# Kernel tuning notes

Measured on AMD Instinct MI355X. Metric: run time of the kernel, lower is better.

The kernel has to match this reference:

```python
import jax, jax.numpy as jnp
import numpy as np

N = 262144  # number of candidate occluded-object feature rows

def _w(k, shape, fan_in):
    return jax.random.normal(k, shape, jnp.float32) * (1.0 / np.sqrt(fan_in))

def setup_inputs() -> dict:
    key = jax.random.key(0)
    ks = jax.random.split(key, 5)
    return {
        "select_feature": jax.random.normal(ks[0], (N, 512), jnp.float32),
        # Conv2d(512,256,1x1) == Linear(512->256); Conv2d(256,128,1x1) == Linear(256->128)
        "W1": _w(ks[1], (256, 512), 512), "b1": jnp.zeros((256,), jnp.float32),
        "W2": _w(ks[2], (128, 256), 256), "b2": jnp.zeros((128,), jnp.float32),
        "Wf1": _w(ks[3], (64, 128), 128), "bf1": jnp.zeros((64,), jnp.float32),
        "Wf2": _w(ks[4], (2, 64), 64),   "bf2": jnp.zeros((2,), jnp.float32),
    }

def reference(select_feature, W1, b1, W2, b2, Wf1, bf1, Wf2, bf2):
    # masker_train: unsqueeze->1x1 convs->squeeze is exactly a per-row MLP.
    h = jax.nn.relu(select_feature @ W1.T + b1)   # [N,256]
    h = jax.nn.relu(h @ W2.T + b2)                # [N,128]
    h = jax.nn.relu(h @ Wf1.T + bf1)              # [N,64]
    logits = h @ Wf2.T + bf2                      # [N,2]
    return jax.nn.softmax(logits, axis=-1)
```

## Files before the change

kernel.cpp:

```cpp
#include <hip/hip_runtime.h>
#include <hip/hip_bf16.h>

typedef __bf16 bf16x8 __attribute__((ext_vector_type(8)));
typedef float  f32x4  __attribute__((ext_vector_type(4)));

#define MFMA16(a, b, c) __builtin_amdgcn_mfma_f32_16x16x32_bf16((a), (b), (c), 0, 0, 0)

__global__ void prep_weights(const float* __restrict__ W1, const float* __restrict__ W2,
                             const float* __restrict__ Wf1, const float* __restrict__ Wf2,
                             __bf16* __restrict__ w1p, __bf16* __restrict__ w2p,
                             __bf16* __restrict__ wf1p, __bf16* __restrict__ wf2b) {
    int t = blockIdx.x * 256 + threadIdx.x;
    int lane = t & 63, m16 = lane & 15, q = (lane >> 4) & 3;
    if (t < 16384) {
        int ct = (t >> 6) & 15, ks = t >> 10;
        const float* s = W1 + (size_t)(ct * 16 + m16) * 512 + ks * 32 + q * 8;
        __bf16* d = w1p + (size_t)t * 8;
        for (int j = 0; j < 8; ++j) d[j] = (__bf16)s[j];
    }
    if (t < 4096) {
        int ct = (t >> 6) & 7, ks = t >> 9;
        const float* s = W2 + (size_t)(ct * 16 + m16) * 256 + ks * 32 + q * 8;
        __bf16* d = w2p + (size_t)t * 8;
        for (int j = 0; j < 8; ++j) d[j] = (__bf16)s[j];
    }
    if (t < 1024) {
        int ct = (t >> 6) & 3, ks = t >> 8;
        const float* s = Wf1 + (size_t)(ct * 16 + m16) * 128 + ks * 32 + q * 8;
        __bf16* d = wf1p + (size_t)t * 8;
        for (int j = 0; j < 8; ++j) d[j] = (__bf16)s[j];
    }
    if (t < 128) wf2b[t] = (__bf16)Wf2[t];
}

__global__ __launch_bounds__(128, 2)
void mlp_kernel(const float* __restrict__ X,
                const __bf16* __restrict__ w1p,  const float* __restrict__ b1,
                const __bf16* __restrict__ w2p,  const float* __restrict__ b2,
                const __bf16* __restrict__ wf1p, const float* __restrict__ bf1,
                const __bf16* __restrict__ wf2b, const float* __restrict__ bf2,
                float* __restrict__ out) {
    __shared__ __align__(16) __bf16 hbuf[2][32][264];

    const int lane = threadIdx.x & 63;
    const int wave = threadIdx.x >> 6;
    const int m16  = lane & 15;
    const int q    = lane >> 4;
    const int row0 = blockIdx.x * 64 + wave * 32;
    __bf16(*hw)[264] = hbuf[wave];

    f32x4 C1[2][16];
#pragma unroll
    for (int rt = 0; rt < 2; ++rt)
#pragma unroll
        for (int ct = 0; ct < 16; ++ct) C1[rt][ct] = (f32x4){0.f, 0.f, 0.f, 0.f};

    const float* xr0 = X + (size_t)(row0 + m16) * 512 + q * 8;
    const float* xr1 = xr0 + (size_t)16 * 512;
    float4 x00 = *(const float4*)(xr0);
    float4 x01 = *(const float4*)(xr0 + 4);
    float4 x10 = *(const float4*)(xr1);
    float4 x11 = *(const float4*)(xr1 + 4);

#pragma unroll
    for (int ks = 0; ks < 16; ++ks) {
        const __bf16* wp = w1p + (size_t)ks * 8192 + lane * 8;
        bf16x8 b0[8], b1v[8];
#pragma unroll
        for (int ct = 0; ct < 8; ++ct)
            b0[ct] = *(const bf16x8*)(wp + ct * 512);

        bf16x8 a0, a1;
        a0[0] = (__bf16)x00.x; a0[1] = (__bf16)x00.y; a0[2] = (__bf16)x00.z; a0[3] = (__bf16)x00.w;
        a0[4] = (__bf16)x01.x; a0[5] = (__bf16)x01.y; a0[6] = (__bf16)x01.z; a0[7] = (__bf16)x01.w;
        a1[0] = (__bf16)x10.x; a1[1] = (__bf16)x10.y; a1[2] = (__bf16)x10.z; a1[3] = (__bf16)x10.w;
        a1[4] = (__bf16)x11.x; a1[5] = (__bf16)x11.y; a1[6] = (__bf16)x11.z; a1[7] = (__bf16)x11.w;

        if (ks < 15) {
            x00 = *(const float4*)(xr0 + (ks + 1) * 32);
            x01 = *(const float4*)(xr0 + (ks + 1) * 32 + 4);
            x10 = *(const float4*)(xr1 + (ks + 1) * 32);
            x11 = *(const float4*)(xr1 + (ks + 1) * 32 + 4);
        }
#pragma unroll
        for (int ct = 0; ct < 8; ++ct)
            b1v[ct] = *(const bf16x8*)(wp + (8 + ct) * 512);

#pragma unroll
        for (int ct = 0; ct < 8; ++ct) {
            C1[0][ct] = MFMA16(a0, b0[ct], C1[0][ct]);
            C1[1][ct] = MFMA16(a1, b0[ct], C1[1][ct]);
        }
#pragma unroll
        for (int ct = 0; ct < 8; ++ct) {
            C1[0][8 + ct] = MFMA16(a0, b1v[ct], C1[0][8 + ct]);
            C1[1][8 + ct] = MFMA16(a1, b1v[ct], C1[1][8 + ct]);
        }
    }
#pragma unroll
    for (int ct = 0; ct < 16; ++ct) {
        float bias = b1[ct * 16 + m16];
#pragma unroll
        for (int rt = 0; rt < 2; ++rt)
#pragma unroll
            for (int r = 0; r < 4; ++r) {
                float v = C1[rt][ct][r] + bias;
                v = v > 0.f ? v : 0.f;
                hw[rt * 16 + q * 4 + r][ct * 16 + m16] = (__bf16)v;
            }
    }

    f32x4 C2[2][8];
#pragma unroll
    for (int rt = 0; rt < 2; ++rt)
#pragma unroll
        for (int ct = 0; ct < 8; ++ct) C2[rt][ct] = (f32x4){0.f, 0.f, 0.f, 0.f};

#pragma unroll
    for (int ks = 0; ks < 8; ++ks) {
        const __bf16* wp = w2p + (size_t)ks * 4096 + lane * 8;
        bf16x8 b[8];
#pragma unroll
        for (int ct = 0; ct < 8; ++ct) b[ct] = *(const bf16x8*)(wp + ct * 512);
        bf16x8 a0 = *(const bf16x8*)&hw[m16][ks * 32 + q * 8];
        bf16x8 a1 = *(const bf16x8*)&hw[16 + m16][ks * 32 + q * 8];
#pragma unroll
        for (int ct = 0; ct < 8; ++ct) {
            C2[0][ct] = MFMA16(a0, b[ct], C2[0][ct]);
            C2[1][ct] = MFMA16(a1, b[ct], C2[1][ct]);
        }
    }
#pragma unroll
    for (int ct = 0; ct < 8; ++ct) {
        float bias = b2[ct * 16 + m16];
#pragma unroll
        for (int rt = 0; rt < 2; ++rt)
#pragma unroll
            for (int r = 0; r < 4; ++r) {
                float v = C2[rt][ct][r] + bias;
                v = v > 0.f ? v : 0.f;
                hw[rt * 16 + q * 4 + r][ct * 16 + m16] = (__bf16)v;
            }
    }

    f32x4 C3[2][4];
#pragma unroll
    for (int rt = 0; rt < 2; ++rt)
#pragma unroll
        for (int ct = 0; ct < 4; ++ct) C3[rt][ct] = (f32x4){0.f, 0.f, 0.f, 0.f};

#pragma unroll
    for (int ks = 0; ks < 4; ++ks) {
        const __bf16* wp = wf1p + (size_t)ks * 2048 + lane * 8;
        bf16x8 b[4];
#pragma unroll
        for (int ct = 0; ct < 4; ++ct) b[ct] = *(const bf16x8*)(wp + ct * 512);
        bf16x8 a0 = *(const bf16x8*)&hw[m16][ks * 32 + q * 8];
        bf16x8 a1 = *(const bf16x8*)&hw[16 + m16][ks * 32 + q * 8];
#pragma unroll
        for (int ct = 0; ct < 4; ++ct) {
            C3[0][ct] = MFMA16(a0, b[ct], C3[0][ct]);
            C3[1][ct] = MFMA16(a1, b[ct], C3[1][ct]);
        }
    }
#pragma unroll
    for (int ct = 0; ct < 4; ++ct) {
        float bias = bf1[ct * 16 + m16];
#pragma unroll
        for (int rt = 0; rt < 2; ++rt)
#pragma unroll
            for (int r = 0; r < 4; ++r) {
                float v = C3[rt][ct][r] + bias;
                v = v > 0.f ? v : 0.f;
                hw[rt * 16 + q * 4 + r][ct * 16 + m16] = (__bf16)v;
            }
    }

    {
        const int r = lane >> 1;
        const int c = lane & 1;
        float dot = 0.f;
#pragma unroll
        for (int j8 = 0; j8 < 8; ++j8) {
            bf16x8 hv = *(const bf16x8*)&hw[r][j8 * 8];
            bf16x8 wv = *(const bf16x8*)(wf2b + c * 64 + j8 * 8);
#pragma unroll
            for (int j = 0; j < 8; ++j) dot += (float)hv[j] * (float)wv[j];
        }
        float logit = dot + bf2[c];
        float other = __shfl_xor(logit, 1, 64);
        float mx = fmaxf(logit, other);
        float e0 = expf(logit - mx);
        float e1 = expf(other - mx);
        out[(size_t)(row0 + r) * 2 + c] = e0 / (e0 + e1);
    }
}

extern "C" void kernel_launch(void* const* d_in, const int* in_sizes, int n_in,
                              void* d_out, int out_size, void* d_ws, size_t ws_size,
                              hipStream_t stream) {
    const float* X   = (const float*)d_in[0];
    const float* W1  = (const float*)d_in[1];
    const float* b1  = (const float*)d_in[2];
    const float* W2  = (const float*)d_in[3];
    const float* b2  = (const float*)d_in[4];
    const float* Wf1 = (const float*)d_in[5];
    const float* bf1 = (const float*)d_in[6];
    const float* Wf2 = (const float*)d_in[7];
    const float* bf2 = (const float*)d_in[8];
    float* out = (float*)d_out;

    const int N = in_sizes[0] / 512;

    __bf16* w1p  = (__bf16*)d_ws;
    __bf16* w2p  = w1p  + 131072;
    __bf16* wf1p = w2p  + 32768;
    __bf16* wf2b = wf1p + 8192;

    prep_weights<<<64, 256, 0, stream>>>(W1, W2, Wf1, Wf2, w1p, w2p, wf1p, wf2b);
    mlp_kernel<<<N / 64, 128, 0, stream>>>(X, w1p, b1, w2p, b2, wf1p, bf1,
                                           wf2b, bf2, out);
}
```

Baseline: 797.9 us.

## Use 4-wave blocks with per-k-step barriers and nontemporal X loads and stores

The block grows from 2 to 4 waves (128 rows), with matching shared memory. An s_barrier is added at every k-step of all three MFMA loops, so the waves stay in lockstep and share the weight fetches in L1/L2. The streaming input loads and the output stores become nontemporal so X does not pollute the cache. The barriers add synchronisation stalls, and launch_bounds(256,2) may tighten the register budget for the large accumulator arrays.

```diff
diff --git a/kernel.cpp b/kernel.cpp
--- a/kernel.cpp
+++ b/kernel.cpp
@@ -5,6 +5,10 @@
 typedef float  f32x4  __attribute__((ext_vector_type(4)));
 
 #define MFMA16(a, b, c) __builtin_amdgcn_mfma_f32_16x16x32_bf16((a), (b), (c), 0, 0, 0)
+
+__device__ __forceinline__ f32x4 nt_load4(const float* p) {
+    return __builtin_nontemporal_load((const f32x4*)p);
+}
 
 __global__ void prep_weights(const float* __restrict__ W1, const float* __restrict__ W2,
                              const float* __restrict__ Wf1, const float* __restrict__ Wf2,
@@ -33,20 +37,20 @@
     if (t < 128) wf2b[t] = (__bf16)Wf2[t];
 }
 
-__global__ __launch_bounds__(128, 2)
+__global__ __launch_bounds__(256, 2)
 void mlp_kernel(const float* __restrict__ X,
                 const __bf16* __restrict__ w1p,  const float* __restrict__ b1,
                 const __bf16* __restrict__ w2p,  const float* __restrict__ b2,
                 const __bf16* __restrict__ wf1p, const float* __restrict__ bf1,
                 const __bf16* __restrict__ wf2b, const float* __restrict__ bf2,
                 float* __restrict__ out) {
-    __shared__ __align__(16) __bf16 hbuf[2][32][264];
+    __shared__ __align__(16) __bf16 hbuf[4][32][264];
 
     const int lane = threadIdx.x & 63;
     const int wave = threadIdx.x >> 6;
     const int m16  = lane & 15;
     const int q    = lane >> 4;
-    const int row0 = blockIdx.x * 64 + wave * 32;
+    const int row0 = blockIdx.x * 128 + wave * 32;
     __bf16(*hw)[264] = hbuf[wave];
 
     f32x4 C1[2][16];
@@ -57,13 +61,14 @@
 
     const float* xr0 = X + (size_t)(row0 + m16) * 512 + q * 8;
     const float* xr1 = xr0 + (size_t)16 * 512;
-    float4 x00 = *(const float4*)(xr0);
-    float4 x01 = *(const float4*)(xr0 + 4);
-    float4 x10 = *(const float4*)(xr1);
-    float4 x11 = *(const float4*)(xr1 + 4);
+    f32x4 x00 = nt_load4(xr0);
+    f32x4 x01 = nt_load4(xr0 + 4);
+    f32x4 x10 = nt_load4(xr1);
+    f32x4 x11 = nt_load4(xr1 + 4);
 
 #pragma unroll
     for (int ks = 0; ks < 16; ++ks) {
+        __builtin_amdgcn_s_barrier();
         const __bf16* wp = w1p + (size_t)ks * 8192 + lane * 8;
         bf16x8 b0[8], b1v[8];
 #pragma unroll
@@ -71,16 +76,16 @@
             b0[ct] = *(const bf16x8*)(wp + ct * 512);
 
         bf16x8 a0, a1;
-        a0[0] = (__bf16)x00.x; a0[1] = (__bf16)x00.y; a0[2] = (__bf16)x00.z; a0[3] = (__bf16)x00.w;
-        a0[4] = (__bf16)x01.x; a0[5] = (__bf16)x01.y; a0[6] = (__bf16)x01.z; a0[7] = (__bf16)x01.w;
-        a1[0] = (__bf16)x10.x; a1[1] = (__bf16)x10.y; a1[2] = (__bf16)x10.z; a1[3] = (__bf16)x10.w;
-        a1[4] = (__bf16)x11.x; a1[5] = (__bf16)x11.y; a1[6] = (__bf16)x11.z; a1[7] = (__bf16)x11.w;
+        a0[0] = (__bf16)x00[0]; a0[1] = (__bf16)x00[1]; a0[2] = (__bf16)x00[2]; a0[3] = (__bf16)x00[3];
+        a0[4] = (__bf16)x01[0]; a0[5] = (__bf16)x01[1]; a0[6] = (__bf16)x01[2]; a0[7] = (__bf16)x01[3];
+        a1[0] = (__bf16)x10[0]; a1[1] = (__bf16)x10[1]; a1[2] = (__bf16)x10[2]; a1[3] = (__bf16)x10[3];
+        a1[4] = (__bf16)x11[0]; a1[5] = (__bf16)x11[1]; a1[6] = (__bf16)x11[2]; a1[7] = (__bf16)x11[3];
 
         if (ks < 15) {
-            x00 = *(const float4*)(xr0 + (ks + 1) * 32);
-            x01 = *(const float4*)(xr0 + (ks + 1) * 32 + 4);
-            x10 = *(const float4*)(xr1 + (ks + 1) * 32);
-            x11 = *(const float4*)(xr1 + (ks + 1) * 32 + 4);
+            x00 = nt_load4(xr0 + (ks + 1) * 32);
+            x01 = nt_load4(xr0 + (ks + 1) * 32 + 4);
+            x10 = nt_load4(xr1 + (ks + 1) * 32);
+            x11 = nt_load4(xr1 + (ks + 1) * 32 + 4);
         }
 #pragma unroll
         for (int ct = 0; ct < 8; ++ct)
@@ -118,6 +123,7 @@
 
 #pragma unroll
     for (int ks = 0; ks < 8; ++ks) {
+        __builtin_amdgcn_s_barrier();
         const __bf16* wp = w2p + (size_t)ks * 4096 + lane * 8;
         bf16x8 b[8];
 #pragma unroll
@@ -151,6 +157,7 @@
 
 #pragma unroll
     for (int ks = 0; ks < 4; ++ks) {
+        __builtin_amdgcn_s_barrier();
         const __bf16* wp = wf1p + (size_t)ks * 2048 + lane * 8;
         bf16x8 b[4];
 #pragma unroll
@@ -192,7 +199,7 @@
         float mx = fmaxf(logit, other);
         float e0 = expf(logit - mx);
         float e1 = expf(other - mx);
-        out[(size_t)(row0 + r) * 2 + c] = e0 / (e0 + e1);
+        __builtin_nontemporal_store(e0 / (e0 + e1), &out[(size_t)(row0 + r) * 2 + c]);
     }
 }
 
@@ -218,6 +225,6 @@
     __bf16* wf2b = wf1p + 8192;
 
     prep_weights<<<64, 256, 0, stream>>>(W1, W2, Wf1, Wf2, w1p, w2p, wf1p, wf2b);
-    mlp_kernel<<<N / 64, 128, 0, stream>>>(X, w1p, b1, w2p, b2, wf1p, bf1,
-                                           wf2b, bf2, out);
-}
+    mlp_kernel<<<N / 128, 256, 0, stream>>>(X, w1p, b1, w2p, b2, wf1p, bf1,
+                                            wf2b, bf2, out);
+}
```

After: 794.1 us. About the same (-0.5%).
